# Performance work log

Hardware: AMD Instinct MI355X
Metric: run time of the kernel (lower is better)

## Reference

```python
import jax, jax.numpy as jnp
import numpy as np

K = 8  # kernel_size
COUT = 512


def setup_inputs() -> dict:
    key = jax.random.key(0)
    k1, k2, k3 = jax.random.split(key, 3)
    B, CIN, L = 8, 512, 2048
    x = jax.random.normal(k1, (B, CIN, L), dtype=jnp.float32)
    # nn.Linear(CIN, COUT*K) weight, scaled like kaiming-uniform-ish init
    W = jax.random.normal(k2, (COUT * K, CIN), dtype=jnp.float32) * (1.0 / np.sqrt(CIN))
    b = jax.random.normal(k3, (COUT,), dtype=jnp.float32)
    return {"x": x, "W": W, "b": b}


def reference(x, W, b):
    # x: (B, Cin, L); W: (Cout*K, Cin) with row layout j = k*Cout + co; b: (Cout,)
    B, Cin, L = x.shape
    # pointwise linear expand: (B, Cout*K, L)
    z = jnp.einsum('bcl,oc->bol', x, W)
    z = z.reshape(B, K, COUT, L)  # k-major channel layout
    # causal overlap-add fold: y[b,co,t] = sum_k z[b,k,co,t-k]
    y = z[:, 0]
    for k in range(1, K):  # small fixed kernel-size loop
        y = y.at[:, :, k:].add(z[:, k, :, : L - k])
    return y + b[None, :, None]
```

## Files before the change

### kernel.cpp

```cpp
#include <hip/hip_runtime.h>
#include <hip/hip_bf16.h>
#include <cstdint>
#include <cstddef>

#define CIN   512
#define COUT  512
#define LLEN  2048
#define BATCH 8
#define KTAP  8
#define LPAD  (LLEN + 8)

typedef __bf16 bf16x8_t __attribute__((ext_vector_type(8)));
typedef float  f32x4_t  __attribute__((ext_vector_type(4)));

__device__ __forceinline__ unsigned short f2bf(float f) {
  __bf16 h = (__bf16)f;
  return __builtin_bit_cast(unsigned short, h);
}

__device__ __forceinline__ void gl2lds16(unsigned short* lds, const unsigned short* g) {
  __builtin_amdgcn_global_load_lds(
      (const __attribute__((address_space(1))) unsigned int*)g,
      (__attribute__((address_space(3))) unsigned int*)lds,
      16, 0, 0);
}


__global__ void zero_pad_kernel(unsigned short* __restrict__ xtp) {
  unsigned short* p = xtp + (size_t)blockIdx.x * LPAD * CIN;
  for (int i = threadIdx.x; i < 8 * CIN; i += 256) p[i] = 0;
}

__global__ void convert_w_kernel(const float4* __restrict__ W, ushort4* __restrict__ Wb) {
  int idx = blockIdx.x * 256 + threadIdx.x;
  float4 v = W[idx];
  ushort4 o;
  o.x = f2bf(v.x); o.y = f2bf(v.y); o.z = f2bf(v.z); o.w = f2bf(v.w);
  Wb[idx] = o;
}

__global__ void transpose_x_kernel(const float* __restrict__ x, unsigned short* __restrict__ xtp) {
  __shared__ float tile[32][33];
  const int b  = blockIdx.z;
  const int c0 = blockIdx.y * 32;
  const int l0 = blockIdx.x * 32;
  const int tx = threadIdx.x & 31, ty = threadIdx.x >> 5;
  const float* xb = x + ((size_t)b * CIN + c0) * LLEN + l0;
#pragma unroll
  for (int i = 0; i < 4; ++i)
    tile[ty + 8 * i][tx] = xb[(size_t)(ty + 8 * i) * LLEN + tx];
  __syncthreads();
  unsigned short* dst = xtp + ((size_t)b * LPAD + 8 + l0) * CIN + c0;
#pragma unroll
  for (int i = 0; i < 4; ++i) {
    int li = ty + 8 * i;
    dst[(size_t)li * CIN + tx] = f2bf(tile[tx][li]);
  }
}


__global__ __launch_bounds__(256) void conv_gemm_kernel(
    const unsigned short* __restrict__ Wb,
    const unsigned short* __restrict__ xtp,
    const float* __restrict__ bias,
    float* __restrict__ y)
{
  __shared__ __align__(16) unsigned short As[128 * 32];
  __shared__ __align__(16) unsigned short Bs[136 * 32];

  const int t    = threadIdx.x;
  const int lane = t & 63;
  const int wid  = t >> 6;
  const int wm   = wid & 1, wn = wid >> 1;
  const int l0   = blockIdx.x * 128;
  const int o0   = blockIdx.y * 128;
  const int b    = blockIdx.z;

  const int quad = lane >> 4;
  const int lrow = lane & 15;

  f32x4_t acc[4][4];
#pragma unroll
  for (int i = 0; i < 4; ++i)
#pragma unroll
    for (int j = 0; j < 4; ++j)
      acc[i][j] = (f32x4_t){0.f, 0.f, 0.f, 0.f};

  const int srow   = t >> 2;
  const int schunk = (t & 3) ^ ((srow >> 1) & 3);
  const int lds_off = t * 8;

  const unsigned short* xb = xtp + (size_t)b * LPAD * CIN;

#pragma unroll 1
  for (int ct = 0; ct < 16; ++ct) {
    const int c0 = ct * 32;
    {
      const unsigned short* src = xb + (size_t)(l0 + srow) * CIN + c0 + schunk * 8;
      gl2lds16(Bs + lds_off, src);
      gl2lds16(Bs + 64 * 32 + lds_off, src + 64 * CIN);
      if (t < 32)
        gl2lds16(Bs + 128 * 32 + lds_off, src + 128 * CIN);
    }
#pragma unroll
    for (int k = 0; k < 8; ++k) {
      const unsigned short* asrc =
          Wb + (size_t)(k * COUT + o0 + srow) * CIN + c0 + schunk * 8;
      gl2lds16(As + lds_off, asrc);
      gl2lds16(As + 64 * 32 + lds_off, asrc + 64 * CIN);
      __syncthreads();

      bf16x8_t af[4], bfr[4];
#pragma unroll
      for (int i = 0; i < 4; ++i) {
        int row = wm * 64 + i * 16 + lrow;
        int off = row * 32 + ((quad ^ ((row >> 1) & 3)) * 8);
        af[i] = *(const bf16x8_t*)(As + off);
      }
#pragma unroll
      for (int j = 0; j < 4; ++j) {
        int row = (8 - k) + wn * 64 + j * 16 + lrow;
        int off = row * 32 + ((quad ^ ((row >> 1) & 3)) * 8);
        bfr[j] = *(const bf16x8_t*)(Bs + off);
      }
#pragma unroll
      for (int i = 0; i < 4; ++i)
#pragma unroll
        for (int j = 0; j < 4; ++j)
          acc[i][j] = __builtin_amdgcn_mfma_f32_16x16x32_bf16(af[i], bfr[j], acc[i][j], 0, 0, 0);
      __syncthreads();
    }
  }

#pragma unroll
  for (int i = 0; i < 4; ++i) {
    const int o_base = o0 + wm * 64 + i * 16 + quad * 4;
    const float4 bv = *(const float4*)(bias + o_base);
    const float bvr[4] = {bv.x, bv.y, bv.z, bv.w};
#pragma unroll
    for (int j = 0; j < 4; ++j) {
      const int l = l0 + wn * 64 + j * 16 + lrow;
#pragma unroll
      for (int r = 0; r < 4; ++r) {
        y[((size_t)b * COUT + o_base + r) * LLEN + l] = acc[i][j][r] + bvr[r];
      }
    }
  }
}


extern "C" void kernel_launch(void* const* d_in, const int* in_sizes, int n_in,
                              void* d_out, int out_size, void* d_ws, size_t ws_size,
                              hipStream_t stream) {
  const float* x    = (const float*)d_in[0];
  const float* W    = (const float*)d_in[1];
  const float* bias = (const float*)d_in[2];
  float* y          = (float*)d_out;

  unsigned short* xtp = (unsigned short*)d_ws;
  unsigned short* Wb  = (unsigned short*)((char*)d_ws +
                        (size_t)BATCH * LPAD * CIN * sizeof(unsigned short));

  zero_pad_kernel<<<BATCH, 256, 0, stream>>>(xtp);
  convert_w_kernel<<<(KTAP * COUT * CIN / 4) / 256, 256, 0, stream>>>(
      (const float4*)W, (ushort4*)Wb);
  transpose_x_kernel<<<dim3(LLEN / 32, CIN / 32, BATCH), 256, 0, stream>>>(x, xtp);
  conv_gemm_kernel<<<dim3(LLEN / 128, COUT / 128, BATCH), 256, 0, stream>>>(
      Wb, xtp, bias, y);
}
```

Before: 161.4 us.

## Double GEMM K-tile to 64, fuse zero-pad into transpose, vectorize prep kernels

The GEMM now stages 64 input channels per tile instead of 32, using an 8-way XOR swizzle, which halves the number of barrier pairs per channel sweep and gives each barrier interval twice the MFMA work. The zero-padding kernel is folded into the transpose kernel, so one launch is removed. The transpose now uses 64x64 tiles with float4 loads and 16-byte bf16 stores. The weight conversion writes 8 bf16 values per thread. The cost is about twice the LDS per block, which may lower occupancy, and the transpose tile reads may have LDS bank conflicts.

```diff
diff --git a/kernel.cpp b/kernel.cpp
--- a/kernel.cpp
+++ b/kernel.cpp
@@ -12,6 +12,7 @@
 
 typedef __bf16 bf16x8_t __attribute__((ext_vector_type(8)));
 typedef float  f32x4_t  __attribute__((ext_vector_type(4)));
+typedef unsigned short u16x8_t __attribute__((ext_vector_type(8)));
 
 __device__ __forceinline__ unsigned short f2bf(float f) {
   __bf16 h = (__bf16)f;
@@ -26,35 +27,52 @@
 }
 
 
-__global__ void zero_pad_kernel(unsigned short* __restrict__ xtp) {
-  unsigned short* p = xtp + (size_t)blockIdx.x * LPAD * CIN;
-  for (int i = threadIdx.x; i < 8 * CIN; i += 256) p[i] = 0;
-}
-
-__global__ void convert_w_kernel(const float4* __restrict__ W, ushort4* __restrict__ Wb) {
+__global__ void convert_w_kernel(const float4* __restrict__ W, u16x8_t* __restrict__ Wb) {
   int idx = blockIdx.x * 256 + threadIdx.x;
-  float4 v = W[idx];
-  ushort4 o;
-  o.x = f2bf(v.x); o.y = f2bf(v.y); o.z = f2bf(v.z); o.w = f2bf(v.w);
+  float4 a = W[idx * 2], b = W[idx * 2 + 1];
+  u16x8_t o;
+  o[0] = f2bf(a.x); o[1] = f2bf(a.y); o[2] = f2bf(a.z); o[3] = f2bf(a.w);
+  o[4] = f2bf(b.x); o[5] = f2bf(b.y); o[6] = f2bf(b.z); o[7] = f2bf(b.w);
   Wb[idx] = o;
 }
 
-__global__ void transpose_x_kernel(const float* __restrict__ x, unsigned short* __restrict__ xtp) {
-  __shared__ float tile[32][33];
+__global__ __launch_bounds__(256) void transpose_x_kernel(
+    const float* __restrict__ x, unsigned short* __restrict__ xtp) {
+  __shared__ float tile[64][65];
+  const int t  = threadIdx.x;
   const int b  = blockIdx.z;
-  const int c0 = blockIdx.y * 32;
-  const int l0 = blockIdx.x * 32;
-  const int tx = threadIdx.x & 31, ty = threadIdx.x >> 5;
-  const float* xb = x + ((size_t)b * CIN + c0) * LLEN + l0;
+  const int c0 = blockIdx.y * 64;
+  const int l0 = blockIdx.x * 64;
+
+  if (blockIdx.x == 0 && t < 64) {
+    unsigned short* hp = xtp + ((size_t)b * LPAD + (t >> 3)) * CIN + c0 + (t & 7) * 8;
+    *(u16x8_t*)hp = (u16x8_t){0, 0, 0, 0, 0, 0, 0, 0};
+  }
+
+  {
+    const int cr = t >> 2;
+    const int lv = (t & 3) * 16;
+    const float* src = x + ((size_t)b * CIN + c0 + cr) * LLEN + l0 + lv;
 #pragma unroll
-  for (int i = 0; i < 4; ++i)
-    tile[ty + 8 * i][tx] = xb[(size_t)(ty + 8 * i) * LLEN + tx];
+    for (int i = 0; i < 4; ++i) {
+      float4 v = *(const float4*)(src + 4 * i);
+      tile[cr][lv + 4 * i + 0] = v.x;
+      tile[cr][lv + 4 * i + 1] = v.y;
+      tile[cr][lv + 4 * i + 2] = v.z;
+      tile[cr][lv + 4 * i + 3] = v.w;
+    }
+  }
   __syncthreads();
-  unsigned short* dst = xtp + ((size_t)b * LPAD + 8 + l0) * CIN + c0;
+
+  {
+    const int l    = t >> 2;
+    const int cseg = (t & 3) * 16;
+    unsigned short ov[16];
 #pragma unroll
-  for (int i = 0; i < 4; ++i) {
-    int li = ty + 8 * i;
-    dst[(size_t)li * CIN + tx] = f2bf(tile[tx][li]);
+    for (int u = 0; u < 16; ++u) ov[u] = f2bf(tile[cseg + u][l]);
+    unsigned short* dst = xtp + ((size_t)b * LPAD + 8 + l0 + l) * CIN + c0 + cseg;
+    *(u16x8_t*)dst       = *(const u16x8_t*)&ov[0];
+    *(u16x8_t*)(dst + 8) = *(const u16x8_t*)&ov[8];
   }
 }
 
@@ -65,8 +83,8 @@
     const float* __restrict__ bias,
     float* __restrict__ y)
 {
-  __shared__ __align__(16) unsigned short As[128 * 32];
-  __shared__ __align__(16) unsigned short Bs[136 * 32];
+  __shared__ __align__(16) unsigned short As[128 * 64];
+  __shared__ __align__(16) unsigned short Bs[136 * 64];
 
   const int t    = threadIdx.x;
   const int lane = t & 63;
@@ -86,48 +104,57 @@
     for (int j = 0; j < 4; ++j)
       acc[i][j] = (f32x4_t){0.f, 0.f, 0.f, 0.f};
 
-  const int srow   = t >> 2;
-  const int schunk = (t & 3) ^ ((srow >> 1) & 3);
+  const int srow    = t >> 3;
+  const int schunk  = (t & 7) ^ (srow & 7);
   const int lds_off = t * 8;
 
   const unsigned short* xb = xtp + (size_t)b * LPAD * CIN;
 
 #pragma unroll 1
-  for (int ct = 0; ct < 16; ++ct) {
-    const int c0 = ct * 32;
+  for (int ct = 0; ct < 8; ++ct) {
+    const int c0 = ct * 64;
     {
       const unsigned short* src = xb + (size_t)(l0 + srow) * CIN + c0 + schunk * 8;
-      gl2lds16(Bs + lds_off, src);
-      gl2lds16(Bs + 64 * 32 + lds_off, src + 64 * CIN);
-      if (t < 32)
-        gl2lds16(Bs + 128 * 32 + lds_off, src + 128 * CIN);
+#pragma unroll
+      for (int rd = 0; rd < 4; ++rd)
+        gl2lds16(Bs + lds_off + rd * 2048, src + (size_t)rd * 32 * CIN);
+      if (t < 64) {
+        const int r2 = 128 + (t >> 3);
+        const int ch2 = (t & 7) ^ (r2 & 7);
+        gl2lds16(Bs + 128 * 64 + t * 8,
+                 xb + (size_t)(l0 + r2) * CIN + c0 + ch2 * 8);
+      }
     }
 #pragma unroll
     for (int k = 0; k < 8; ++k) {
       const unsigned short* asrc =
           Wb + (size_t)(k * COUT + o0 + srow) * CIN + c0 + schunk * 8;
-      gl2lds16(As + lds_off, asrc);
-      gl2lds16(As + 64 * 32 + lds_off, asrc + 64 * CIN);
+#pragma unroll
+      for (int rd = 0; rd < 4; ++rd)
+        gl2lds16(As + lds_off + rd * 2048, asrc + (size_t)rd * 32 * CIN);
       __syncthreads();
 
-      bf16x8_t af[4], bfr[4];
 #pragma unroll
-      for (int i = 0; i < 4; ++i) {
-        int row = wm * 64 + i * 16 + lrow;
-        int off = row * 32 + ((quad ^ ((row >> 1) & 3)) * 8);
-        af[i] = *(const bf16x8_t*)(As + off);
+      for (int h = 0; h < 2; ++h) {
+        bf16x8_t af[4], bfr[4];
+#pragma unroll
+        for (int i = 0; i < 4; ++i) {
+          int row  = wm * 64 + i * 16 + lrow;
+          int slot = (h * 4 + quad) ^ (row & 7);
+          af[i] = *(const bf16x8_t*)(As + row * 64 + slot * 8);
+        }
+#pragma unroll
+        for (int j = 0; j < 4; ++j) {
+          int row  = (8 - k) + wn * 64 + j * 16 + lrow;
+          int slot = (h * 4 + quad) ^ (row & 7);
+          bfr[j] = *(const bf16x8_t*)(Bs + row * 64 + slot * 8);
+        }
+#pragma unroll
+        for (int i = 0; i < 4; ++i)
+#pragma unroll
+          for (int j = 0; j < 4; ++j)
+            acc[i][j] = __builtin_amdgcn_mfma_f32_16x16x32_bf16(af[i], bfr[j], acc[i][j], 0, 0, 0);
       }
-#pragma unroll
-      for (int j = 0; j < 4; ++j) {
-        int row = (8 - k) + wn * 64 + j * 16 + lrow;
-        int off = row * 32 + ((quad ^ ((row >> 1) & 3)) * 8);
-        bfr[j] = *(const bf16x8_t*)(Bs + off);
-      }
-#pragma unroll
-      for (int i = 0; i < 4; ++i)
-#pragma unroll
-        for (int j = 0; j < 4; ++j)
-          acc[i][j] = __builtin_amdgcn_mfma_f32_16x16x32_bf16(af[i], bfr[j], acc[i][j], 0, 0, 0);
       __syncthreads();
     }
   }
@@ -161,10 +188,9 @@
   unsigned short* Wb  = (unsigned short*)((char*)d_ws +
                         (size_t)BATCH * LPAD * CIN * sizeof(unsigned short));
 
-  zero_pad_kernel<<<BATCH, 256, 0, stream>>>(xtp);
-  convert_w_kernel<<<(KTAP * COUT * CIN / 4) / 256, 256, 0, stream>>>(
-      (const float4*)W, (ushort4*)Wb);
-  transpose_x_kernel<<<dim3(LLEN / 32, CIN / 32, BATCH), 256, 0, stream>>>(x, xtp);
+  convert_w_kernel<<<(KTAP * COUT * CIN / 8) / 256, 256, 0, stream>>>(
+      (const float4*)W, (u16x8_t*)Wb);
+  transpose_x_kernel<<<dim3(LLEN / 64, CIN / 64, BATCH), 256, 0, stream>>>(x, xtp);
   conv_gemm_kernel<<<dim3(LLEN / 128, COUT / 128, BATCH), 256, 0, stream>>>(
       Wb, xtp, bias, y);
 }
```

Result: faster. 150.0 us (-7.1%).
